# Kernel tuning notes

Hardware: AMD Instinct MI355X
Metric: run time of the kernel (lower is better)

## Reference

```python
import jax, jax.numpy as jnp
import numpy as np

N = 100000
E = 1600000
D = 64        # HID_NODE_ENC == HID_EDGE_ENC
H = 128       # HIDDEN_NODE_ONE
EPS = 1e-5
NEG_SLOPE = 0.01


def _xavier(key, shape):
    fan_in, fan_out = shape[0], shape[1]
    limit = float(np.sqrt(6.0 / (fan_in + fan_out)))
    return jax.random.uniform(key, shape, jnp.float32, -limit, limit)


def setup_inputs() -> dict:
    key = jax.random.key(0)
    ks = jax.random.split(key, 10)
    x = jax.random.normal(ks[0], (N, D), jnp.float32)
    edge_index = jax.random.randint(ks[1], (2, E), 0, N, jnp.int64)
    edge_attr = jax.random.normal(ks[2], (E, D), jnp.float32)
    u = jax.random.normal(ks[3], (1, 16), jnp.float32)
    batch = jnp.zeros((N,), jnp.int64)
    b_init = jnp.float32(0.01)
    params = {
        # node_mlp_1: Lin(128->128), LeakyReLU, BN(128), Lin(128->128)
        "W1": _xavier(ks[4], (2 * D, H)), "b1": jnp.full((H,), b_init),
        "g1": jnp.ones((H,), jnp.float32), "be1": jnp.zeros((H,), jnp.float32),
        "W2": _xavier(ks[5], (H, H)), "b2": jnp.full((H,), b_init),
        # node_mlp_2: Lin(192->128), LeakyReLU, BN(128), Lin(128->64)
        "W3": _xavier(ks[6], (H + D, H)), "b3": jnp.full((H,), b_init),
        "g2": jnp.ones((H,), jnp.float32), "be2": jnp.zeros((H,), jnp.float32),
        "W4": _xavier(ks[7], (H, D)), "b4": jnp.full((D,), b_init),
    }
    return {"x": x, "edge_index": edge_index, "edge_attr": edge_attr,
            "u": u, "batch": batch, **params}


def _bn(h, gamma, beta):
    # BatchNorm1d in training mode: biased batch statistics
    mean = jnp.mean(h, axis=0)
    var = jnp.mean(jnp.square(h - mean), axis=0)
    return (h - mean) * jax.lax.rsqrt(var + EPS) * gamma + beta


def reference(x, edge_index, edge_attr, u, batch,
              W1, b1, g1, be1, W2, b2,
              W3, b3, g2, be2, W4, b4):
    row, col = edge_index[0], edge_index[1]
    # gather + concat: [E, 2D]
    h = jnp.concatenate([x[row], edge_attr], axis=1)
    # node_mlp_1
    h = jax.nn.leaky_relu(h @ W1 + b1, NEG_SLOPE)
    h = _bn(h, g1, be1)
    h = h @ W2 + b2                       # [E, H]
    # scatter_add by destination node
    agg = jax.ops.segment_sum(h, col, num_segments=x.shape[0])  # [N, H]
    # concat with node feats, node_mlp_2
    h2 = jnp.concatenate([x, agg], axis=1)  # [N, H+D]
    h2 = jax.nn.leaky_relu(h2 @ W3 + b3, NEG_SLOPE)
    h2 = _bn(h2, g2, be2)
    return h2 @ W4 + b4                    # [N, D]
```

## Files before the change

### kernel.cpp

```cpp
#include <hip/hip_runtime.h>

#define NN 100000
#define NE 1600000
#define NTILE_E (NE / 128)
#define NTILE_N 782

typedef __attribute__((ext_vector_type(4))) float f32x4;
typedef __attribute__((ext_vector_type(8))) short s16x8;

__device__ __forceinline__ unsigned short f2bf(float f) {
  unsigned u = __builtin_bit_cast(unsigned, f);
  u = (u + 0x7FFFu + ((u >> 16) & 1u)) >> 16;
  return (unsigned short)u;
}
__device__ __forceinline__ void pack4(float4 v, unsigned short* dst) {
  ushort4 h;
  h.x = f2bf(v.x); h.y = f2bf(v.y); h.z = f2bf(v.z); h.w = f2bf(v.w);
  *(ushort4*)dst = h;
}

__global__ void k0_prep(const float* __restrict__ W1, const float* __restrict__ W3,
                        unsigned short* __restrict__ W1bT, unsigned short* __restrict__ W3bT) {
  int i = blockIdx.x * 256 + threadIdx.x;
  if (i < 16384) {
    int n = i >> 7, k = i & 127;
    W1bT[i] = f2bf(W1[k * 128 + n]);
  } else if (i < 16384 + 24576) {
    int j = i - 16384;
    int n = j / 192, k = j % 192;
    W3bT[j] = f2bf(W3[k * 128 + n]);
  }
}

__global__ void k_hist(const int* __restrict__ eidx, int* __restrict__ hist) {
  int e = blockIdx.x * 256 + threadIdx.x;
  if (e < NE) atomicAdd(&hist[eidx[NE + e]], 1);
}

__global__ void k_scan(int* __restrict__ hist, float* __restrict__ cntF) {
  __shared__ int ssum[1024];
  const int t = threadIdx.x;
  const int base = t * 98;
  const int cl = (base >= NN) ? 0 : ((NN - base < 98) ? (NN - base) : 98);
  int s = 0;
  for (int i = 0; i < cl; i++) s += hist[base + i];
  ssum[t] = s;
  __syncthreads();
  for (int d = 1; d < 1024; d <<= 1) {
    int v = (t >= d) ? ssum[t - d] : 0;
    __syncthreads();
    ssum[t] += v;
    __syncthreads();
  }
  int run = (t == 0) ? 0 : ssum[t - 1];
  for (int i = 0; i < cl; i++) {
    int hv = hist[base + i];
    hist[base + i] = run;
    cntF[base + i] = (float)hv;
    run += hv;
  }
}

__global__ void k_scatter(const int* __restrict__ eidx, int* __restrict__ off,
                          int2* __restrict__ pairS) {
  int e = blockIdx.x * 256 + threadIdx.x;
  if (e < NE) {
    int c = eidx[NE + e];
    int p = atomicAdd(&off[c], 1);
    pairS[p] = make_int2(c, e);
  }
}

__global__ __launch_bounds__(512, 4) void k1_edge(
    const float* __restrict__ x, const int* __restrict__ eidx,
    const float* __restrict__ ea, const unsigned short* __restrict__ W1bT,
    const float* __restrict__ b1, const int2* __restrict__ pairS,
    float* __restrict__ S, float* __restrict__ stat1) {
  __shared__ __align__(16) char HAt[67584];
  __shared__ int rIdxS[128];
  __shared__ int eIdxS[128];
  __shared__ int colT[132];
  __shared__ float sred[256];
  unsigned short (*At)[136] = (unsigned short (*)[136])HAt;
  float (*H)[132] = (float (*)[132])HAt;

  const int tid = threadIdx.x;
  const int wave = tid >> 6, lane = tid & 63;
  const int l15 = lane & 15, quad = lane >> 4;
  const int rowbase = (wave >> 1) * 32;
  const int colbase = (wave & 1) * 64;

  s16x8 bfrag[4][4];
#pragma unroll
  for (int ct = 0; ct < 4; ct++)
#pragma unroll
    for (int ks = 0; ks < 4; ks++)
      bfrag[ct][ks] = *(const s16x8*)(W1bT + (colbase + ct * 16 + l15) * 128 + ks * 32 + quad * 8);

  float b1j[4];
#pragma unroll
  for (int ct = 0; ct < 4; ct++) b1j[ct] = b1[colbase + ct * 16 + l15];

  float lsum[4] = {0, 0, 0, 0}, lsq[4] = {0, 0, 0, 0};

  for (int tile = blockIdx.x; tile < NTILE_E; tile += gridDim.x) {
    const int eb = tile * 128;
    __syncthreads();
    if (tid < 128) {
      int2 pr = pairS[eb + tid];
      eIdxS[tid] = pr.y;
      rIdxS[tid] = eidx[pr.y];
      colT[tid + 1] = pr.x;
    } else if (tid == 128) {
      colT[0] = (eb > 0) ? pairS[eb - 1].x : -1;
    } else if (tid == 129) {
      colT[129] = (eb + 128 < NE) ? pairS[eb + 128].x : -1;
    }
    __syncthreads();
#pragma unroll
    for (int i = 0; i < 4; i++) {
      int idx = tid + i * 512; int e = idx >> 4, c = idx & 15;
      float4 v = ((const float4*)x)[(size_t)rIdxS[e] * 16 + c];
      pack4(v, &At[e][c * 4]);
    }
#pragma unroll
    for (int i = 0; i < 4; i++) {
      int idx = tid + i * 512; int e = idx >> 4, c = idx & 15;
      float4 v = ((const float4*)ea)[(size_t)eIdxS[e] * 16 + c];
      pack4(v, &At[e][64 + c * 4]);
    }
    __syncthreads();

    f32x4 acc[2][4];
#pragma unroll
    for (int rt = 0; rt < 2; rt++)
#pragma unroll
      for (int ct = 0; ct < 4; ct++) acc[rt][ct] = (f32x4){0.f, 0.f, 0.f, 0.f};

#pragma unroll
    for (int ks = 0; ks < 4; ks++) {
      s16x8 af[2];
#pragma unroll
      for (int rt = 0; rt < 2; rt++)
        af[rt] = *(const s16x8*)&At[rowbase + rt * 16 + l15][ks * 32 + quad * 8];
#pragma unroll
      for (int rt = 0; rt < 2; rt++)
#pragma unroll
        for (int ct = 0; ct < 4; ct++)
          acc[rt][ct] = __builtin_amdgcn_mfma_f32_16x16x32_bf16(af[rt], bfrag[ct][ks], acc[rt][ct], 0, 0, 0);
    }

    __syncthreads();
#pragma unroll
    for (int rt = 0; rt < 2; rt++)
#pragma unroll
      for (int r = 0; r < 4; r++) {
        const int er = rowbase + rt * 16 + quad * 4 + r;
#pragma unroll
        for (int ct = 0; ct < 4; ct++) {
          float v = acc[rt][ct][r] + b1j[ct];
          v = v > 0.0f ? v : 0.01f * v;
          lsum[ct] += v; lsq[ct] += v * v;
          H[er][colbase + ct * 16 + l15] = v;
        }
      }
    __syncthreads();

    {
      const int col = tid & 127;
      const int r0 = (tid >> 7) * 32;
      float runsum = H[r0][col];
      int runstart = r0;
      int curnode = colT[r0 + 1];
      for (int r = r0 + 1; r < r0 + 32; ++r) {
        int nd = colT[r + 1];
        float v = H[r][col];
        if (nd == curnode) { runsum += v; }
        else {
          float* p = S + (size_t)curnode * 128 + col;
          if (colT[runstart] != curnode) *p = runsum;
          else atomicAdd(p, runsum);
          curnode = nd; runsum = v; runstart = r;
        }
      }
      float* p = S + (size_t)curnode * 128 + col;
      if (colT[runstart] != curnode && colT[r0 + 33] != curnode) *p = runsum;
      else atomicAdd(p, runsum);
    }
  }

  if (tid < 256) sred[tid] = 0.0f;
  __syncthreads();
#pragma unroll
  for (int ct = 0; ct < 4; ct++) {
    float s = lsum[ct], q = lsq[ct];
    s += __shfl_down(s, 32); q += __shfl_down(q, 32);
    s += __shfl_down(s, 16); q += __shfl_down(q, 16);
    if (lane < 16) {
      atomicAdd(&sred[colbase + ct * 16 + l15], s);
      atomicAdd(&sred[128 + colbase + ct * 16 + l15], q);
    }
  }
  __syncthreads();
  if (tid < 256) atomicAdd(&stat1[tid], sred[tid]);
}

__global__ void k2_fold1(const float* __restrict__ stat1, const float* __restrict__ g1,
                         const float* __restrict__ be1, const float* __restrict__ W2,
                         const float* __restrict__ b2,
                         unsigned short* __restrict__ W2pT, float* __restrict__ v128) {
  __shared__ float s1s[128], t1s[128];
  __shared__ float red[256];
  const int tid = threadIdx.x;
  if (tid < 128) {
    float mean = stat1[tid] * (1.0f / NE);
    float var = stat1[128 + tid] * (1.0f / NE) - mean * mean;
    float rstd = rsqrtf(var + 1e-5f);
    float s = g1[tid] * rstd;
    s1s[tid] = s; t1s[tid] = be1[tid] - mean * s;
  }
  __syncthreads();
  const int b = blockIdx.x;
  if (b < 16) {
#pragma unroll
    for (int j = 0; j < 4; j++) {
      int i = b * 1024 + j * 256 + tid;
      int k = i >> 7, n = i & 127;
      W2pT[n * 128 + k] = f2bf(s1s[k] * W2[i]);
    }
  } else {
    int j = tid & 127, hh = tid >> 7;
    float p = 0.f;
    for (int k = hh * 64; k < hh * 64 + 64; k++) p += t1s[k] * W2[k * 128 + j];
    red[tid] = p;
    __syncthreads();
    if (tid < 128) v128[tid] = red[tid] + red[tid + 128] + b2[tid];
  }
}

__global__ __launch_bounds__(256, 3) void k3_node(
    const float* __restrict__ x, const float* __restrict__ S, const float* __restrict__ cnt,
    const unsigned short* __restrict__ W2pT, const float* __restrict__ v128,
    const unsigned short* __restrict__ W3bT, const float* __restrict__ b3,
    unsigned short* __restrict__ tOut, float* __restrict__ stat2) {
  __shared__ __align__(16) unsigned short Abuf[128][200];
  __shared__ float cbuf[128];
  __shared__ float sred[256];

  const int tid = threadIdx.x;
  const int wave = tid >> 6, lane = tid & 63;
  const int l15 = lane & 15, quad = lane >> 4;
  const int rowbase = (wave >> 1) * 64;
  const int colbase = (wave & 1) * 64;

  float vj[4], b3j[4];
#pragma unroll
  for (int ct = 0; ct < 4; ct++) {
    int jc = colbase + ct * 16 + l15;
    vj[ct] = v128[jc]; b3j[ct] = b3[jc];
  }
  float lsum[4] = {0, 0, 0, 0}, lsq[4] = {0, 0, 0, 0};

  for (int t = blockIdx.x; t < NTILE_N; t += gridDim.x) {
    const int nb = t * 128;
    __syncthreads();
#pragma unroll
    for (int i = 0; i < 8; i++) {
      int idx = tid + i * 256; int e = idx >> 4, c = idx & 15;
      int node = nb + e;
      float4 v = {0.f, 0.f, 0.f, 0.f};
      if (node < NN) v = ((const float4*)x)[(size_t)node * 16 + c];
      pack4(v, &Abuf[e][c * 4]);
    }
#pragma unroll
    for (int i = 0; i < 16; i++) {
      int idx = tid + i * 256; int e = idx >> 5, c = idx & 31;
      int node = nb + e;
      float4 v = {0.f, 0.f, 0.f, 0.f};
      if (node < NN) v = ((const float4*)S)[(size_t)node * 32 + c];
      pack4(v, &Abuf[e][64 + c * 4]);
    }
    if (tid < 128) cbuf[tid] = (nb + tid < NN) ? cnt[nb + tid] : 0.0f;
    __syncthreads();

    f32x4 acc[4][4];
#pragma unroll
    for (int rt = 0; rt < 4; rt++)
#pragma unroll
      for (int ct = 0; ct < 4; ct++) acc[rt][ct] = (f32x4){0.f, 0.f, 0.f, 0.f};
#pragma unroll
    for (int ks = 0; ks < 4; ks++) {
      s16x8 af[4];
#pragma unroll
      for (int rt = 0; rt < 4; rt++)
        af[rt] = *(const s16x8*)&Abuf[rowbase + rt * 16 + l15][64 + ks * 32 + quad * 8];
      s16x8 bfr[4];
#pragma unroll
      for (int ct = 0; ct < 4; ct++)
        bfr[ct] = *(const s16x8*)(W2pT + (colbase + ct * 16 + l15) * 128 + ks * 32 + quad * 8);
#pragma unroll
      for (int rt = 0; rt < 4; rt++)
#pragma unroll
        for (int ct = 0; ct < 4; ct++)
          acc[rt][ct] = __builtin_amdgcn_mfma_f32_16x16x32_bf16(af[rt], bfr[ct], acc[rt][ct], 0, 0, 0);
    }
    __syncthreads();
#pragma unroll
    for (int rt = 0; rt < 4; rt++)
#pragma unroll
      for (int r = 0; r < 4; r++) {
        int er = rowbase + rt * 16 + quad * 4 + r;
#pragma unroll
        for (int ct = 0; ct < 4; ct++) {
          float val = acc[rt][ct][r] + cbuf[er] * vj[ct];
          Abuf[er][64 + colbase + ct * 16 + l15] = f2bf(val);
        }
      }
    __syncthreads();

    f32x4 acc2[4][4];
#pragma unroll
    for (int rt = 0; rt < 4; rt++)
#pragma unroll
      for (int ct = 0; ct < 4; ct++) acc2[rt][ct] = (f32x4){0.f, 0.f, 0.f, 0.f};
#pragma unroll
    for (int ks = 0; ks < 6; ks++) {
      s16x8 af[4];
#pragma unroll
      for (int rt = 0; rt < 4; rt++)
        af[rt] = *(const s16x8*)&Abuf[rowbase + rt * 16 + l15][ks * 32 + quad * 8];
      s16x8 bfr[4];
#pragma unroll
      for (int ct = 0; ct < 4; ct++)
        bfr[ct] = *(const s16x8*)(W3bT + (size_t)(colbase + ct * 16 + l15) * 192 + ks * 32 + quad * 8);
#pragma unroll
      for (int rt = 0; rt < 4; rt++)
#pragma unroll
        for (int ct = 0; ct < 4; ct++)
          acc2[rt][ct] = __builtin_amdgcn_mfma_f32_16x16x32_bf16(af[rt], bfr[ct], acc2[rt][ct], 0, 0, 0);
    }

#pragma unroll
    for (int rt = 0; rt < 4; rt++)
#pragma unroll
      for (int r = 0; r < 4; r++) {
        int er = rowbase + rt * 16 + quad * 4 + r;
        int node = nb + er;
        if (node < NN) {
#pragma unroll
          for (int ct = 0; ct < 4; ct++) {
            float val = acc2[rt][ct][r] + b3j[ct];
            val = val > 0.0f ? val : 0.01f * val;
            lsum[ct] += val; lsq[ct] += val * val;
            tOut[(size_t)node * 128 + colbase + ct * 16 + l15] = f2bf(val);
          }
        }
      }
  }

  sred[tid] = 0.0f;
  __syncthreads();
#pragma unroll
  for (int ct = 0; ct < 4; ct++) {
    float s = lsum[ct], q = lsq[ct];
    s += __shfl_down(s, 32); q += __shfl_down(q, 32);
    s += __shfl_down(s, 16); q += __shfl_down(q, 16);
    if (lane < 16) {
      atomicAdd(&sred[colbase + ct * 16 + l15], s);
      atomicAdd(&sred[128 + colbase + ct * 16 + l15], q);
    }
  }
  __syncthreads();
  atomicAdd(&stat2[tid], sred[tid]);
}

__global__ void k5_fold2(const float* __restrict__ stat2, const float* __restrict__ g2,
                         const float* __restrict__ be2, const float* __restrict__ W4,
                         const float* __restrict__ b4,
                         unsigned short* __restrict__ W4fT, float* __restrict__ b4f) {
  __shared__ float s2s[128], t2s[128];
  __shared__ float red[256];
  const int tid = threadIdx.x;
  if (tid < 128) {
    float mean = stat2[tid] * (1.0f / NN);
    float var = stat2[128 + tid] * (1.0f / NN) - mean * mean;
    float rstd = rsqrtf(var + 1e-5f);
    float s = g2[tid] * rstd;
    s2s[tid] = s; t2s[tid] = be2[tid] - mean * s;
  }
  __syncthreads();
  const int b = blockIdx.x;
  if (b < 8) {
#pragma unroll
    for (int j = 0; j < 4; j++) {
      int i = b * 1024 + j * 256 + tid;
      int k = i >> 6, n = i & 63;
      W4fT[n * 128 + k] = f2bf(s2s[k] * W4[i]);
    }
  } else {
    int j = tid & 63, part = tid >> 6;
    float p = 0.f;
    for (int k = part * 32; k < part * 32 + 32; k++) p += t2s[k] * W4[k * 64 + j];
    red[tid] = p;
    __syncthreads();
    if (tid < 64) b4f[tid] = red[tid] + red[tid + 64] + red[tid + 128] + red[tid + 192] + b4[tid];
  }
}

__global__ __launch_bounds__(256, 4) void k6_out(
    const unsigned short* __restrict__ tIn, const unsigned short* __restrict__ W4fT,
    const float* __restrict__ b4f, float* __restrict__ out) {
  __shared__ unsigned short Abuf[128][136];
  const int tid = threadIdx.x;
  const int wave = tid >> 6, lane = tid & 63;
  const int l15 = lane & 15, quad = lane >> 4;
  const int rowbase = (wave >> 1) * 64;
  const int colbase = (wave & 1) * 32;

  s16x8 bfrag[2][4];
#pragma unroll
  for (int ct = 0; ct < 2; ct++)
#pragma unroll
    for (int ks = 0; ks < 4; ks++)
      bfrag[ct][ks] = *(const s16x8*)(W4fT + (colbase + ct * 16 + l15) * 128 + ks * 32 + quad * 8);
  float bj[2];
#pragma unroll
  for (int ct = 0; ct < 2; ct++) bj[ct] = b4f[colbase + ct * 16 + l15];

  for (int t = blockIdx.x; t < NTILE_N; t += gridDim.x) {
    const int nb = t * 128;
    __syncthreads();
#pragma unroll
    for (int i = 0; i < 8; i++) {
      int idx = tid + i * 256; int e = idx >> 4, c = idx & 15;
      int node = nb + e;
      s16x8 v = {0, 0, 0, 0, 0, 0, 0, 0};
      if (node < NN) v = *(const s16x8*)(tIn + (size_t)node * 128 + c * 8);
      *(s16x8*)&Abuf[e][c * 8] = v;
    }
    __syncthreads();

    f32x4 acc[4][2];
#pragma unroll
    for (int rt = 0; rt < 4; rt++)
#pragma unroll
      for (int ct = 0; ct < 2; ct++) acc[rt][ct] = (f32x4){0.f, 0.f, 0.f, 0.f};
#pragma unroll
    for (int ks = 0; ks < 4; ks++) {
      s16x8 af[4];
#pragma unroll
      for (int rt = 0; rt < 4; rt++)
        af[rt] = *(const s16x8*)&Abuf[rowbase + rt * 16 + l15][ks * 32 + quad * 8];
#pragma unroll
      for (int rt = 0; rt < 4; rt++)
#pragma unroll
        for (int ct = 0; ct < 2; ct++)
          acc[rt][ct] = __builtin_amdgcn_mfma_f32_16x16x32_bf16(af[rt], bfrag[ct][ks], acc[rt][ct], 0, 0, 0);
    }
#pragma unroll
    for (int rt = 0; rt < 4; rt++)
#pragma unroll
      for (int r = 0; r < 4; r++) {
        int er = rowbase + rt * 16 + quad * 4 + r;
        int node = nb + er;
        if (node < NN) {
#pragma unroll
          for (int ct = 0; ct < 2; ct++)
            out[(size_t)node * 64 + colbase + ct * 16 + l15] = acc[rt][ct][r] + bj[ct];
        }
      }
  }
}

extern "C" void kernel_launch(void* const* d_in, const int* in_sizes, int n_in,
                              void* d_out, int out_size, void* d_ws, size_t ws_size,
                              hipStream_t stream) {
  (void)in_sizes; (void)n_in; (void)out_size; (void)ws_size;
  const float* x   = (const float*)d_in[0];
  const int*   ei  = (const int*)d_in[1];
  const float* ea  = (const float*)d_in[2];
  const float* W1  = (const float*)d_in[5];
  const float* b1  = (const float*)d_in[6];
  const float* g1  = (const float*)d_in[7];
  const float* be1 = (const float*)d_in[8];
  const float* W2  = (const float*)d_in[9];
  const float* b2  = (const float*)d_in[10];
  const float* W3  = (const float*)d_in[11];
  const float* b3  = (const float*)d_in[12];
  const float* g2  = (const float*)d_in[13];
  const float* be2 = (const float*)d_in[14];
  const float* W4  = (const float*)d_in[15];
  const float* b4  = (const float*)d_in[16];
  float* out = (float*)d_out;

  char* w = (char*)d_ws;
  float* S     = (float*)(w);
  float* stat1 = (float*)(w + 51200000);
  float* stat2 = (float*)(w + 51201024);
  int*   hist  = (int*)  (w + 51202048);
  float* cntF  = (float*)(w + 51602432);
  unsigned short* W1bT = (unsigned short*)(w + 52002816);
  unsigned short* W3bT = (unsigned short*)(w + 52035584);
  unsigned short* W2pT = (unsigned short*)(w + 52084736);
  float* v128  = (float*)(w + 52117504);
  unsigned short* W4fT = (unsigned short*)(w + 52118016);
  float* b4f   = (float*)(w + 52134400);
  unsigned short* tOut = (unsigned short*)(w + 52134656);
  int2* pairS = (int2*)(w + 52134656);

  hipMemsetAsync(d_ws, 0, 51602432, stream);

  k0_prep<<<160, 256, 0, stream>>>(W1, W3, W1bT, W3bT);
  k_hist<<<6250, 256, 0, stream>>>(ei, hist);
  k_scan<<<1, 1024, 0, stream>>>(hist, cntF);
  k_scatter<<<6250, 256, 0, stream>>>(ei, hist, pairS);
  k1_edge<<<512, 512, 0, stream>>>(x, ei, ea, W1bT, b1, pairS, S, stat1);
  k2_fold1<<<17, 256, 0, stream>>>(stat1, g1, be1, W2, b2, W2pT, v128);
  k3_node<<<512, 256, 0, stream>>>(x, S, cntF, W2pT, v128, W3bT, b3, tOut, stat2);
  k5_fold2<<<9, 256, 0, stream>>>(stat2, g2, be2, W4, b4, W4fT, b4f);
  k6_out<<<512, 256, 0, stream>>>(tOut, W4fT, b4f, out);
}
```

Measured before the change: 1.414 ms.

## Prefetch next edge tile indices, rebalance edge wave tiling, split node LDS buffers

```diff
diff --git a/kernel.cpp b/kernel.cpp
--- a/kernel.cpp
+++ b/kernel.cpp
@@ -71,15 +71,16 @@
   }
 }
 
-__global__ __launch_bounds__(512, 4) void k1_edge(
+__global__ __attribute__((amdgpu_flat_work_group_size(512, 512)))
+__attribute__((amdgpu_waves_per_eu(4))) void k1_edge(
     const float* __restrict__ x, const int* __restrict__ eidx,
     const float* __restrict__ ea, const unsigned short* __restrict__ W1bT,
     const float* __restrict__ b1, const int2* __restrict__ pairS,
     float* __restrict__ S, float* __restrict__ stat1) {
   __shared__ __align__(16) char HAt[67584];
-  __shared__ int rIdxS[128];
-  __shared__ int eIdxS[128];
-  __shared__ int colT[132];
+  __shared__ int rIdx2[2][128];
+  __shared__ int eIdx2[2][128];
+  __shared__ int colT2[2][132];
   __shared__ float sred[256];
   unsigned short (*At)[136] = (unsigned short (*)[136])HAt;
   float (*H)[132] = (float (*)[132])HAt;
@@ -87,77 +88,96 @@
   const int tid = threadIdx.x;
   const int wave = tid >> 6, lane = tid & 63;
   const int l15 = lane & 15, quad = lane >> 4;
-  const int rowbase = (wave >> 1) * 32;
-  const int colbase = (wave & 1) * 64;
-
-  s16x8 bfrag[4][4];
-#pragma unroll
-  for (int ct = 0; ct < 4; ct++)
+  const int rowbase = (wave >> 2) * 64;
+  const int colbase = (wave & 3) * 32;
+
+  s16x8 bfrag[2][4];
+#pragma unroll
+  for (int ct = 0; ct < 2; ct++)
 #pragma unroll
     for (int ks = 0; ks < 4; ks++)
       bfrag[ct][ks] = *(const s16x8*)(W1bT + (colbase + ct * 16 + l15) * 128 + ks * 32 + quad * 8);
 
-  float b1j[4];
-#pragma unroll
-  for (int ct = 0; ct < 4; ct++) b1j[ct] = b1[colbase + ct * 16 + l15];
-
-  float lsum[4] = {0, 0, 0, 0}, lsq[4] = {0, 0, 0, 0};
-
-  for (int tile = blockIdx.x; tile < NTILE_E; tile += gridDim.x) {
-    const int eb = tile * 128;
-    __syncthreads();
+  float b1j[2];
+#pragma unroll
+  for (int ct = 0; ct < 2; ct++) b1j[ct] = b1[colbase + ct * 16 + l15];
+
+  float lsum[2] = {0, 0}, lsq[2] = {0, 0};
+
+  {
+    const int eb = blockIdx.x * 128;
     if (tid < 128) {
       int2 pr = pairS[eb + tid];
-      eIdxS[tid] = pr.y;
-      rIdxS[tid] = eidx[pr.y];
-      colT[tid + 1] = pr.x;
+      eIdx2[0][tid] = pr.y;
+      rIdx2[0][tid] = eidx[pr.y];
+      colT2[0][tid + 1] = pr.x;
     } else if (tid == 128) {
-      colT[0] = (eb > 0) ? pairS[eb - 1].x : -1;
+      colT2[0][0] = (eb > 0) ? pairS[eb - 1].x : -1;
     } else if (tid == 129) {
-      colT[129] = (eb + 128 < NE) ? pairS[eb + 128].x : -1;
-    }
+      colT2[0][129] = (eb + 128 < NE) ? pairS[eb + 128].x : -1;
+    }
+  }
+
+  int p = 0;
+  for (int tile = blockIdx.x; tile < NTILE_E; tile += gridDim.x) {
     __syncthreads();
 #pragma unroll
     for (int i = 0; i < 4; i++) {
       int idx = tid + i * 512; int e = idx >> 4, c = idx & 15;
-      float4 v = ((const float4*)x)[(size_t)rIdxS[e] * 16 + c];
+      float4 v = ((const float4*)x)[(size_t)rIdx2[p][e] * 16 + c];
       pack4(v, &At[e][c * 4]);
     }
 #pragma unroll
     for (int i = 0; i < 4; i++) {
       int idx = tid + i * 512; int e = idx >> 4, c = idx & 15;
-      float4 v = ((const float4*)ea)[(size_t)eIdxS[e] * 16 + c];
+      float4 v = ((const float4*)ea)[(size_t)eIdx2[p][e] * 16 + c];
       pack4(v, &At[e][64 + c * 4]);
     }
-    __syncthreads();
-
-    f32x4 acc[2][4];
-#pragma unroll
-    for (int rt = 0; rt < 2; rt++)
-#pragma unroll
-      for (int ct = 0; ct < 4; ct++) acc[rt][ct] = (f32x4){0.f, 0.f, 0.f, 0.f};
+    {
+      const int ntile = tile + gridDim.x;
+      if (ntile < NTILE_E) {
+        const int eb2 = ntile * 128;
+        if (tid < 128) {
+          int2 pr = pairS[eb2 + tid];
+          eIdx2[p ^ 1][tid] = pr.y;
+          rIdx2[p ^ 1][tid] = eidx[pr.y];
+          colT2[p ^ 1][tid + 1] = pr.x;
+        } else if (tid == 128) {
+          colT2[p ^ 1][0] = pairS[eb2 - 1].x;
+        } else if (tid == 129) {
+          colT2[p ^ 1][129] = (eb2 + 128 < NE) ? pairS[eb2 + 128].x : -1;
+        }
+      }
+    }
+    __syncthreads();
+
+    f32x4 acc[4][2];
+#pragma unroll
+    for (int rt = 0; rt < 4; rt++)
+#pragma unroll
+      for (int ct = 0; ct < 2; ct++) acc[rt][ct] = (f32x4){0.f, 0.f, 0.f, 0.f};
 
 #pragma unroll
     for (int ks = 0; ks < 4; ks++) {
-      s16x8 af[2];
-#pragma unroll
-      for (int rt = 0; rt < 2; rt++)
+      s16x8 af[4];
+#pragma unroll
+      for (int rt = 0; rt < 4; rt++)
         af[rt] = *(const s16x8*)&At[rowbase + rt * 16 + l15][ks * 32 + quad * 8];
 #pragma unroll
-      for (int rt = 0; rt < 2; rt++)
-#pragma unroll
-        for (int ct = 0; ct < 4; ct++)
+      for (int rt = 0; rt < 4; rt++)
+#pragma unroll
+        for (int ct = 0; ct < 2; ct++)
           acc[rt][ct] = __builtin_amdgcn_mfma_f32_16x16x32_bf16(af[rt], bfrag[ct][ks], acc[rt][ct], 0, 0, 0);
     }
 
     __syncthreads();
 #pragma unroll
-    for (int rt = 0; rt < 2; rt++)
+    for (int rt = 0; rt < 4; rt++)
 #pragma unroll
       for (int r = 0; r < 4; r++) {
         const int er = rowbase + rt * 16 + quad * 4 + r;
 #pragma unroll
-        for (int ct = 0; ct < 4; ct++) {
+        for (int ct = 0; ct < 2; ct++) {
           float v = acc[rt][ct][r] + b1j[ct];
           v = v > 0.0f ? v : 0.01f * v;
           lsum[ct] += v; lsq[ct] += v * v;
@@ -171,28 +191,29 @@
       const int r0 = (tid >> 7) * 32;
       float runsum = H[r0][col];
       int runstart = r0;
-      int curnode = colT[r0 + 1];
+      int curnode = colT2[p][r0 + 1];
       for (int r = r0 + 1; r < r0 + 32; ++r) {
-        int nd = colT[r + 1];
+        int nd = colT2[p][r + 1];
         float v = H[r][col];
         if (nd == curnode) { runsum += v; }
         else {
-          float* p = S + (size_t)curnode * 128 + col;
-          if (colT[runstart] != curnode) *p = runsum;
-          else atomicAdd(p, runsum);
+          float* pp = S + (size_t)curnode * 128 + col;
+          if (colT2[p][runstart] != curnode) *pp = runsum;
+          else atomicAdd(pp, runsum);
           curnode = nd; runsum = v; runstart = r;
         }
       }
-      float* p = S + (size_t)curnode * 128 + col;
-      if (colT[runstart] != curnode && colT[r0 + 33] != curnode) *p = runsum;
-      else atomicAdd(p, runsum);
-    }
+      float* pp = S + (size_t)curnode * 128 + col;
+      if (colT2[p][runstart] != curnode && colT2[p][r0 + 33] != curnode) *pp = runsum;
+      else atomicAdd(pp, runsum);
+    }
+    p ^= 1;
   }
 
   if (tid < 256) sred[tid] = 0.0f;
   __syncthreads();
 #pragma unroll
-  for (int ct = 0; ct < 4; ct++) {
+  for (int ct = 0; ct < 2; ct++) {
     float s = lsum[ct], q = lsq[ct];
     s += __shfl_down(s, 32); q += __shfl_down(q, 32);
     s += __shfl_down(s, 16); q += __shfl_down(q, 16);
@@ -238,12 +259,13 @@
   }
 }
 
-__global__ __launch_bounds__(256, 3) void k3_node(
+__global__ __launch_bounds__(256, 2) void k3_node(
     const float* __restrict__ x, const float* __restrict__ S, const float* __restrict__ cnt,
     const unsigned short* __restrict__ W2pT, const float* __restrict__ v128,
     const unsigned short* __restrict__ W3bT, const float* __restrict__ b3,
     unsigned short* __restrict__ tOut, float* __restrict__ stat2) {
-  __shared__ __align__(16) unsigned short Abuf[128][200];
+  __shared__ unsigned short Abuf[128][136];
+  __shared__ unsigned short Xbuf[128][72];
   __shared__ float cbuf[128];
   __shared__ float sred[256];
 
@@ -265,20 +287,20 @@
     const int nb = t * 128;
     __syncthreads();
 #pragma unroll
+    for (int i = 0; i < 16; i++) {
+      int idx = tid + i * 256; int e = idx >> 5, c = idx & 31;
+      int node = nb + e;
+      float4 v = {0.f, 0.f, 0.f, 0.f};
+      if (node < NN) v = ((const float4*)S)[(size_t)node * 32 + c];
+      pack4(v, &Abuf[e][c * 4]);
+    }
+#pragma unroll
     for (int i = 0; i < 8; i++) {
       int idx = tid + i * 256; int e = idx >> 4, c = idx & 15;
       int node = nb + e;
       float4 v = {0.f, 0.f, 0.f, 0.f};
       if (node < NN) v = ((const float4*)x)[(size_t)node * 16 + c];
-      pack4(v, &Abuf[e][c * 4]);
-    }
-#pragma unroll
-    for (int i = 0; i < 16; i++) {
-      int idx = tid + i * 256; int e = idx >> 5, c = idx & 31;
-      int node = nb + e;
-      float4 v = {0.f, 0.f, 0.f, 0.f};
-      if (node < NN) v = ((const float4*)S)[(size_t)node * 32 + c];
-      pack4(v, &Abuf[e][64 + c * 4]);
+      pack4(v, &Xbuf[e][c * 4]);
     }
     if (tid < 128) cbuf[tid] = (nb + tid < NN) ? cnt[nb + tid] : 0.0f;
     __syncthreads();
@@ -293,7 +315,7 @@
       s16x8 af[4];
 #pragma unroll
       for (int rt = 0; rt < 4; rt++)
-        af[rt] = *(const s16x8*)&Abuf[rowbase + rt * 16 + l15][64 + ks * 32 + quad * 8];
+        af[rt] = *(const s16x8*)&Abuf[rowbase + rt * 16 + l15][ks * 32 + quad * 8];
       s16x8 bfr[4];
 #pragma unroll
       for (int ct = 0; ct < 4; ct++)
@@ -313,7 +335,7 @@
 #pragma unroll
         for (int ct = 0; ct < 4; ct++) {
           float val = acc[rt][ct][r] + cbuf[er] * vj[ct];
-          Abuf[er][64 + colbase + ct * 16 + l15] = f2bf(val);
+          Abuf[er][colbase + ct * 16 + l15] = f2bf(val);
         }
       }
     __syncthreads();
@@ -326,9 +348,15 @@
 #pragma unroll
     for (int ks = 0; ks < 6; ks++) {
       s16x8 af[4];
-#pragma unroll
-      for (int rt = 0; rt < 4; rt++)
-        af[rt] = *(const s16x8*)&Abuf[rowbase + rt * 16 + l15][ks * 32 + quad * 8];
+      if (ks < 2) {
+#pragma unroll
+        for (int rt = 0; rt < 4; rt++)
+          af[rt] = *(const s16x8*)&Xbuf[rowbase + rt * 16 + l15][ks * 32 + quad * 8];
+      } else {
+#pragma unroll
+        for (int rt = 0; rt < 4; rt++)
+          af[rt] = *(const s16x8*)&Abuf[rowbase + rt * 16 + l15][(ks - 2) * 32 + quad * 8];
+      }
       s16x8 bfr[4];
 #pragma unroll
       for (int ct = 0; ct < 4; ct++)
@@ -407,7 +435,7 @@
   }
 }
 
-__global__ __launch_bounds__(256, 4) void k6_out(
+__global__ __launch_bounds__(256, 2) void k6_out(
     const unsigned short* __restrict__ tIn, const unsigned short* __restrict__ W4fT,
     const float* __restrict__ b4f, float* __restrict__ out) {
   __shared__ unsigned short Abuf[128][136];
```

Result: faster. 1.209 ms (-14.5%).
